# Performance work log

Measured on AMD Instinct MI355X. Metric: run time of the kernel, lower is better.

Reference implementation:

```python
import jax, jax.numpy as jnp
import numpy as np

B, H, S, D = 2, 16, 2048, 128


def setup_inputs() -> dict:
    key = jax.random.key(0)
    kq, kk, kv, km = jax.random.split(key, 4)
    query = jax.random.normal(kq, (B, H, S, D), dtype=jnp.float32)
    k_ = jax.random.normal(kk, (B, H, S, D), dtype=jnp.float32)
    value = jax.random.normal(kv, (B, H, S, D), dtype=jnp.float32)
    # per-sample context mask (attn_mask * learned mask scalar -> continuous floats)
    ctx_mask = jax.random.uniform(km, (B, S), dtype=jnp.float32)
    return {"query": query, "key": k_, "value": value, "ctx_mask": ctx_mask}


def reference(query, key, value, ctx_mask):
    # Faithful port of the monkey-patched GPT-Neo _attn (eval mode, no
    # attention_mask / head_mask, dropout = identity).
    q = query.astype(jnp.float32)
    k = key.astype(jnp.float32)
    # GPT-Neo: no 1/sqrt(d) scaling
    scores = jnp.einsum("bhqd,bhkd->bhqk", q, k)  # [B,H,S,S] fp32
    q_len, k_len = scores.shape[-2], scores.shape[-1]
    causal = jnp.tril(jnp.ones((q_len, k_len), dtype=bool))  # bias buffer slice
    mask_value = jnp.finfo(scores.dtype).min
    scores = jnp.where(causal, scores, mask_value)
    attn = jax.nn.softmax(scores, axis=-1).astype(value.dtype)
    # per-sample ctx_mask multiply over the key axis (post-softmax!)
    attn = attn * ctx_mask[:, None, None, :]
    out = jnp.einsum("bhqk,bhkd->bhqd", attn, value)
    return out
```

## Files before the change

### kernel.cpp

```cpp
#include <hip/hip_runtime.h>
#include <stdint.h>


#define S_LEN 2048
#define DIM 128
#define QTILE 128
#define KTILE 32
#define LOG2E 1.44269504088896340736f
#define NEG_BIG (-3.0e38f)

typedef _Float16 half8 __attribute__((ext_vector_type(8)));
typedef float f32x16 __attribute__((ext_vector_type(16)));

union U4H8 { uint4 u; half8 h; };

static __device__ __forceinline__ unsigned int pkh2(float a, float b) {
  unsigned short ua = __builtin_bit_cast(unsigned short, (_Float16)a);
  unsigned short ub = __builtin_bit_cast(unsigned short, (_Float16)b);
  return (unsigned int)ua | ((unsigned int)ub << 16);
}

static __device__ __forceinline__ void split8(const float* x, uint4& uh, uint4& ul) {
  unsigned int h[4], l[4];
#pragma unroll
  for (int i = 0; i < 4; ++i) {
    float a = x[2 * i], b = x[2 * i + 1];
    _Float16 ha = (_Float16)a, hb = (_Float16)b;
    float ra = a - (float)ha, rb = b - (float)hb;
    h[i] = (unsigned int)__builtin_bit_cast(unsigned short, ha)
         | ((unsigned int)__builtin_bit_cast(unsigned short, hb) << 16);
    l[i] = (unsigned int)__builtin_bit_cast(unsigned short, (_Float16)ra)
         | ((unsigned int)__builtin_bit_cast(unsigned short, (_Float16)rb) << 16);
  }
  uh = make_uint4(h[0], h[1], h[2], h[3]);
  ul = make_uint4(l[0], l[1], l[2], l[3]);
}

__global__ __launch_bounds__(256, 2) void attn_fwd(
    const float* __restrict__ Q, const float* __restrict__ K,
    const float* __restrict__ V, const float* __restrict__ CM,
    float* __restrict__ O) {
  __shared__ uint4 sKhi[512];
  __shared__ uint4 sKlo[512];
  __shared__ uint4 sVt[512];

  const int tid = (int)threadIdx.x;
  const int lane = tid & 63;
  const int wv = tid >> 6;
  const int l31 = lane & 31;
  const int hif = lane >> 5;

  const int pid = (int)blockIdx.x;
  const int t16 = pid >> 5;
  const int qt = (t16 < 8) ? t16 : (23 - t16);
  const int bh = pid & 31;
  const int b = bh >> 4;

  const float* Qb = Q + (size_t)bh * (S_LEN * DIM);
  const float* Kb = K + (size_t)bh * (S_LEN * DIM);
  const float* Vb = V + (size_t)bh * (S_LEN * DIM);
  const float* CMb = CM + (size_t)b * S_LEN;
  float* Ob = O + (size_t)bh * (S_LEN * DIM);

  const int qb = qt * QTILE + wv * 32;
  const int q = qb + l31;
  const int kdiag = qb >> 5;
  const int nkt = 4 * qt + 4;

  uint4 qh[8], ql[8];
  {
    const float* qrow = Qb + (size_t)q * DIM;
#pragma unroll
    for (int ko = 0; ko < 8; ++ko) {
      const int d0 = ko * 16 + hif * 8;
      float4 f0 = *(const float4*)(qrow + d0);
      float4 f1 = *(const float4*)(qrow + d0 + 4);
      float x[8] = {f0.x * LOG2E, f0.y * LOG2E, f0.z * LOG2E, f0.w * LOG2E,
                    f1.x * LOG2E, f1.y * LOG2E, f1.z * LOG2E, f1.w * LOG2E};
      split8(x, qh[ko], ql[ko]);
    }
  }

  f32x16 accO[4];
#pragma unroll
  for (int dt = 0; dt < 4; ++dt)
#pragma unroll
    for (int i = 0; i < 16; ++i) accO[dt][i] = 0.f;
  float m = NEG_BIG;
  float lsum = 0.f;

  for (int kt = 0; kt < nkt; ++kt) {
    __syncthreads();
    const int kb = kt * KTILE;

#pragma unroll
    for (int cc = 0; cc < 2; ++cc) {
      const int c = tid + cc * 256;
      const int row = c >> 4;
      const int col8 = c & 15;
      const float* src = Kb + (size_t)(kb + row) * DIM + col8 * 8;
      float4 f0 = *(const float4*)src;
      float4 f1 = *(const float4*)(src + 4);
      float x[8] = {f0.x, f0.y, f0.z, f0.w, f1.x, f1.y, f1.z, f1.w};
      uint4 uh, ul;
      split8(x, uh, ul);
      const int idx = row * 16 + (col8 ^ (row & 7));
      sKhi[idx] = uh;
      sKlo[idx] = ul;
    }
#pragma unroll
    for (int cc = 0; cc < 2; ++cc) {
      const int c = tid + cc * 256;
      const int kc = c >> 7;
      const int d = c & 127;
      unsigned int pk[4];
#pragma unroll
      for (int i = 0; i < 4; ++i) {
        const int k0 = kb + kc * 8 + 2 * i;
        float a = Vb[(size_t)k0 * DIM + d] * CMb[k0];
        float bb = Vb[(size_t)(k0 + 1) * DIM + d] * CMb[k0 + 1];
        pk[i] = pkh2(a, bb);
      }
      sVt[c] = make_uint4(pk[0], pk[1], pk[2], pk[3]);
    }
    __syncthreads();

    if (kt > kdiag) continue;

    f32x16 s;
#pragma unroll
    for (int i = 0; i < 16; ++i) s[i] = 0.f;
    const int rbase = l31 * 16;
    const int sw = l31 & 7;
#pragma unroll
    for (int ko = 0; ko < 8; ++ko) {
      const int idx = rbase + ((2 * ko + hif) ^ sw);
      U4H8 ah, al, bhq, blq;
      ah.u = sKhi[idx];
      al.u = sKlo[idx];
      bhq.u = qh[ko];
      blq.u = ql[ko];
      s = __builtin_amdgcn_mfma_f32_32x32x16_f16(al.h, bhq.h, s, 0, 0, 0);
      s = __builtin_amdgcn_mfma_f32_32x32x16_f16(ah.h, blq.h, s, 0, 0, 0);
      s = __builtin_amdgcn_mfma_f32_32x32x16_f16(ah.h, bhq.h, s, 0, 0, 0);
    }

    if (kt == kdiag) {
#pragma unroll
      for (int r = 0; r < 16; ++r) {
        const int crow = (r & 3) + 8 * (r >> 2) + 4 * hif;
        if (crow > l31) s[r] = NEG_BIG;
      }
    }

    float pmax = s[0];
#pragma unroll
    for (int r = 1; r < 16; ++r) pmax = fmaxf(pmax, s[r]);
    pmax = fmaxf(pmax, __shfl_xor(pmax, 32));

    if (__any(pmax > m + 8.0f)) {
      const float mnew = fmaxf(m, pmax);
      const float sc = exp2f(m - mnew);
      m = mnew;
      lsum *= sc;
#pragma unroll
      for (int dt = 0; dt < 4; ++dt)
#pragma unroll
        for (int i = 0; i < 16; ++i) accO[dt][i] *= sc;
    }

    float p[16];
    float psum = 0.f;
#pragma unroll
    for (int r = 0; r < 16; ++r) {
      p[r] = exp2f(s[r] - m);
      psum += p[r];
    }
    psum += __shfl_xor(psum, 32);
    lsum += psum;

#pragma unroll
    for (int ko = 0; ko < 2; ++ko) {
      const unsigned int a0 = pkh2(p[8 * ko + 0], p[8 * ko + 1]);
      const unsigned int a1 = pkh2(p[8 * ko + 2], p[8 * ko + 3]);
      const unsigned int b0 = pkh2(p[8 * ko + 4], p[8 * ko + 5]);
      const unsigned int b1 = pkh2(p[8 * ko + 6], p[8 * ko + 7]);
      const unsigned int s0 = hif ? a0 : b0;
      const unsigned int s1 = hif ? a1 : b1;
      const unsigned int r0 = __shfl_xor(s0, 32);
      const unsigned int r1 = __shfl_xor(s1, 32);
      U4H8 pf;
      if (hif) pf.u = make_uint4(r0, r1, b0, b1);
      else     pf.u = make_uint4(a0, a1, r0, r1);
#pragma unroll
      for (int dt = 0; dt < 4; ++dt) {
        U4H8 vf;
        vf.u = sVt[(2 * ko + hif) * 128 + dt * 32 + l31];
        accO[dt] = __builtin_amdgcn_mfma_f32_32x32x16_f16(vf.h, pf.h, accO[dt], 0, 0, 0);
      }
    }
  }

  const float rinv = 1.0f / lsum;
  float* orow = Ob + (size_t)q * DIM;
#pragma unroll
  for (int dt = 0; dt < 4; ++dt) {
#pragma unroll
    for (int g = 0; g < 4; ++g) {
      float4 o;
      o.x = accO[dt][4 * g + 0] * rinv;
      o.y = accO[dt][4 * g + 1] * rinv;
      o.z = accO[dt][4 * g + 2] * rinv;
      o.w = accO[dt][4 * g + 3] * rinv;
      *(float4*)(orow + dt * 32 + g * 8 + 4 * hif) = o;
    }
  }
}

extern "C" void kernel_launch(void* const* d_in, const int* in_sizes, int n_in,
                              void* d_out, int out_size, void* d_ws, size_t ws_size,
                              hipStream_t stream) {
  const float* Q = (const float*)d_in[0];
  const float* K = (const float*)d_in[1];
  const float* V = (const float*)d_in[2];
  const float* CM = (const float*)d_in[3];
  float* Out = (float*)d_out;
  hipLaunchKernelGGL(attn_fwd, dim3(512), dim3(256), 0, stream, Q, K, V, CM, Out);
}
```

Before: 295.1 us.

## Prepack K/V tiles in workspace and double-buffer async loads into LDS

Adds a prepack kernel that splits K into hi/lo fp16 and multiplies V by ctx_mask, transposing it to fp16, once per tile into a workspace. The attention kernel then streams the prepacked tiles into double-buffered LDS with global_load_lds while computing, and raises wave priority around the MFMA blocks. Each query-tile block no longer repeats the conversion work, and the loads overlap with compute. In exchange it adds an extra kernel launch, a workspace round trip through HBM, and double the LDS per block. It falls back to the old kernel if the workspace is too small.

```diff
diff --git a/kernel.cpp b/kernel.cpp
--- a/kernel.cpp
+++ b/kernel.cpp
@@ -6,11 +6,17 @@
 #define DIM 128
 #define QTILE 128
 #define KTILE 32
+#define NKT_TOT 64
+#define TILE_U4 1536
+#define WS_NEED ((size_t)32 * NKT_TOT * TILE_U4 * 16)
 #define LOG2E 1.44269504088896340736f
 #define NEG_BIG (-3.0e38f)
 
 typedef _Float16 half8 __attribute__((ext_vector_type(8)));
 typedef float f32x16 __attribute__((ext_vector_type(16)));
+typedef unsigned int u32;
+typedef __attribute__((address_space(3))) u32 lds_u32;
+typedef const __attribute__((address_space(1))) u32 glb_u32;
 
 union U4H8 { uint4 u; half8 h; };
 
@@ -36,13 +42,61 @@
   ul = make_uint4(l[0], l[1], l[2], l[3]);
 }
 
-__global__ __launch_bounds__(256, 2) void attn_fwd(
-    const float* __restrict__ Q, const float* __restrict__ K,
-    const float* __restrict__ V, const float* __restrict__ CM,
+__global__ __launch_bounds__(256) void prepack(
+    const float* __restrict__ K, const float* __restrict__ V,
+    const float* __restrict__ CM, uint4* __restrict__ ws) {
+  const int bid = (int)blockIdx.x;
+  const int bh = bid >> 6;
+  const int kt = bid & 63;
+  const int b = bh >> 4;
+  const int kb = kt * KTILE;
+  const int tid = (int)threadIdx.x;
+  const float* Kb = K + (size_t)bh * (S_LEN * DIM);
+  const float* Vb = V + (size_t)bh * (S_LEN * DIM);
+  const float* CMb = CM + (size_t)b * S_LEN;
+  uint4* tile = ws + (size_t)bid * TILE_U4;
+
+#pragma unroll
+  for (int cc = 0; cc < 2; ++cc) {
+    const int c = tid + cc * 256;
+    const int row = c >> 4;
+    const int col8 = c & 15;
+    const float* src = Kb + (size_t)(kb + row) * DIM + col8 * 8;
+    float4 f0 = *(const float4*)src;
+    float4 f1 = *(const float4*)(src + 4);
+    float x[8] = {f0.x, f0.y, f0.z, f0.w, f1.x, f1.y, f1.z, f1.w};
+    uint4 uh, ul;
+    split8(x, uh, ul);
+    const int idx = row * 16 + (col8 ^ (row & 7));
+    tile[idx] = uh;
+    tile[512 + idx] = ul;
+  }
+
+  const int kc = tid >> 6;
+  const int half = (tid >> 5) & 1;
+  const int dgrp = tid & 31;
+  const int k0 = kb + kc * 8 + half * 4;
+  float cm[4];
+  float vv[4][4];
+#pragma unroll
+  for (int j = 0; j < 4; ++j) {
+    cm[j] = CMb[k0 + j];
+    *(float4*)vv[j] = *(const float4*)(Vb + (size_t)(k0 + j) * DIM + dgrp * 4);
+  }
+#pragma unroll
+  for (int i = 0; i < 4; ++i) {
+    uint2 w;
+    w.x = pkh2(vv[0][i] * cm[0], vv[1][i] * cm[1]);
+    w.y = pkh2(vv[2][i] * cm[2], vv[3][i] * cm[3]);
+    char* dst = (char*)(tile + 1024 + kc * 128 + dgrp * 4 + i) + half * 8;
+    *(uint2*)dst = w;
+  }
+}
+
+__global__ __launch_bounds__(256, 2) void attn_fwd2(
+    const float* __restrict__ Q, const uint4* __restrict__ ws,
     float* __restrict__ O) {
-  __shared__ uint4 sKhi[512];
-  __shared__ uint4 sKlo[512];
-  __shared__ uint4 sVt[512];
+  __shared__ uint4 sBuf[2][TILE_U4];
 
   const int tid = (int)threadIdx.x;
   const int lane = tid & 63;
@@ -54,18 +108,24 @@
   const int t16 = pid >> 5;
   const int qt = (t16 < 8) ? t16 : (23 - t16);
   const int bh = pid & 31;
-  const int b = bh >> 4;
 
   const float* Qb = Q + (size_t)bh * (S_LEN * DIM);
-  const float* Kb = K + (size_t)bh * (S_LEN * DIM);
-  const float* Vb = V + (size_t)bh * (S_LEN * DIM);
-  const float* CMb = CM + (size_t)b * S_LEN;
   float* Ob = O + (size_t)bh * (S_LEN * DIM);
+  const uint4* wsbh = ws + (size_t)bh * NKT_TOT * TILE_U4;
 
   const int qb = qt * QTILE + wv * 32;
   const int q = qb + l31;
   const int kdiag = qb >> 5;
   const int nkt = 4 * qt + 4;
+
+  {
+    const uint4* src = wsbh;
+#pragma unroll
+    for (int j = 0; j < 6; ++j) {
+      __builtin_amdgcn_global_load_lds((glb_u32*)(src + tid + j * 256),
+                                       (lds_u32*)&sBuf[0][tid + j * 256], 16, 0, 0);
+    }
+  }
 
   uint4 qh[8], ql[8];
   {
@@ -89,10 +149,174 @@
   float m = NEG_BIG;
   float lsum = 0.f;
 
+  __syncthreads();
+
+  int cur = 0;
+  for (int kt = 0; kt < nkt; ++kt) {
+    if (kt + 1 < nkt) {
+      const uint4* src = wsbh + (size_t)(kt + 1) * TILE_U4;
+#pragma unroll
+      for (int j = 0; j < 6; ++j) {
+        __builtin_amdgcn_global_load_lds((glb_u32*)(src + tid + j * 256),
+                                         (lds_u32*)&sBuf[cur ^ 1][tid + j * 256], 16, 0, 0);
+      }
+    }
+
+    if (kt <= kdiag) {
+      f32x16 s;
+#pragma unroll
+      for (int i = 0; i < 16; ++i) s[i] = 0.f;
+      const int rbase = l31 * 16;
+      const int sw = l31 & 7;
+      __builtin_amdgcn_s_setprio(1);
+#pragma unroll
+      for (int ko = 0; ko < 8; ++ko) {
+        const int idx = rbase + ((2 * ko + hif) ^ sw);
+        U4H8 ah, al, bhq, blq;
+        ah.u = sBuf[cur][idx];
+        al.u = sBuf[cur][512 + idx];
+        bhq.u = qh[ko];
+        blq.u = ql[ko];
+        s = __builtin_amdgcn_mfma_f32_32x32x16_f16(al.h, bhq.h, s, 0, 0, 0);
+        s = __builtin_amdgcn_mfma_f32_32x32x16_f16(ah.h, blq.h, s, 0, 0, 0);
+        s = __builtin_amdgcn_mfma_f32_32x32x16_f16(ah.h, bhq.h, s, 0, 0, 0);
+      }
+      __builtin_amdgcn_s_setprio(0);
+
+      if (kt == kdiag) {
+#pragma unroll
+        for (int r = 0; r < 16; ++r) {
+          const int crow = (r & 3) + 8 * (r >> 2) + 4 * hif;
+          if (crow > l31) s[r] = NEG_BIG;
+        }
+      }
+
+      float pmax = s[0];
+#pragma unroll
+      for (int r = 1; r < 16; ++r) pmax = fmaxf(pmax, s[r]);
+      pmax = fmaxf(pmax, __shfl_xor(pmax, 32));
+
+      if (__any(pmax > m + 8.0f)) {
+        const float mnew = fmaxf(m, pmax);
+        const float sc = exp2f(m - mnew);
+        m = mnew;
+        lsum *= sc;
+#pragma unroll
+        for (int dt = 0; dt < 4; ++dt)
+#pragma unroll
+          for (int i = 0; i < 16; ++i) accO[dt][i] *= sc;
+      }
+
+      float p[16];
+      float psum = 0.f;
+#pragma unroll
+      for (int r = 0; r < 16; ++r) {
+        p[r] = exp2f(s[r] - m);
+        psum += p[r];
+      }
+      psum += __shfl_xor(psum, 32);
+      lsum += psum;
+
+      __builtin_amdgcn_s_setprio(1);
+#pragma unroll
+      for (int ko = 0; ko < 2; ++ko) {
+        const unsigned int a0 = pkh2(p[8 * ko + 0], p[8 * ko + 1]);
+        const unsigned int a1 = pkh2(p[8 * ko + 2], p[8 * ko + 3]);
+        const unsigned int b0 = pkh2(p[8 * ko + 4], p[8 * ko + 5]);
+        const unsigned int b1 = pkh2(p[8 * ko + 6], p[8 * ko + 7]);
+        const unsigned int s0 = hif ? a0 : b0;
+        const unsigned int s1 = hif ? a1 : b1;
+        const unsigned int r0 = __shfl_xor(s0, 32);
+        const unsigned int r1 = __shfl_xor(s1, 32);
+        U4H8 pf;
+        if (hif) pf.u = make_uint4(r0, r1, b0, b1);
+        else     pf.u = make_uint4(a0, a1, r0, r1);
+#pragma unroll
+        for (int dt = 0; dt < 4; ++dt) {
+          U4H8 vf;
+          vf.u = sBuf[cur][1024 + (2 * ko + hif) * 128 + dt * 32 + l31];
+          accO[dt] = __builtin_amdgcn_mfma_f32_32x32x16_f16(vf.h, pf.h, accO[dt], 0, 0, 0);
+        }
+      }
+      __builtin_amdgcn_s_setprio(0);
+    }
+
+    __syncthreads();
+    cur ^= 1;
+  }
+
+  const float rinv = 1.0f / lsum;
+  float* orow = Ob + (size_t)q * DIM;
+#pragma unroll
+  for (int dt = 0; dt < 4; ++dt) {
+#pragma unroll
+    for (int g = 0; g < 4; ++g) {
+      float4 o;
+      o.x = accO[dt][4 * g + 0] * rinv;
+      o.y = accO[dt][4 * g + 1] * rinv;
+      o.z = accO[dt][4 * g + 2] * rinv;
+      o.w = accO[dt][4 * g + 3] * rinv;
+      *(float4*)(orow + dt * 32 + g * 8 + 4 * hif) = o;
+    }
+  }
+}
+
+__global__ __launch_bounds__(256, 2) void attn_fwd_fb(
+    const float* __restrict__ Q, const float* __restrict__ K,
+    const float* __restrict__ V, const float* __restrict__ CM,
+    float* __restrict__ O) {
+  __shared__ uint4 sKhi[512];
+  __shared__ uint4 sKlo[512];
+  __shared__ uint4 sVt[512];
+
+  const int tid = (int)threadIdx.x;
+  const int lane = tid & 63;
+  const int wv = tid >> 6;
+  const int l31 = lane & 31;
+  const int hif = lane >> 5;
+
+  const int pid = (int)blockIdx.x;
+  const int t16 = pid >> 5;
+  const int qt = (t16 < 8) ? t16 : (23 - t16);
+  const int bh = pid & 31;
+  const int b = bh >> 4;
+
+  const float* Qb = Q + (size_t)bh * (S_LEN * DIM);
+  const float* Kb = K + (size_t)bh * (S_LEN * DIM);
+  const float* Vb = V + (size_t)bh * (S_LEN * DIM);
+  const float* CMb = CM + (size_t)b * S_LEN;
+  float* Ob = O + (size_t)bh * (S_LEN * DIM);
+
+  const int qb = qt * QTILE + wv * 32;
+  const int q = qb + l31;
+  const int kdiag = qb >> 5;
+  const int nkt = 4 * qt + 4;
+
+  uint4 qh[8], ql[8];
+  {
+    const float* qrow = Qb + (size_t)q * DIM;
+#pragma unroll
+    for (int ko = 0; ko < 8; ++ko) {
+      const int d0 = ko * 16 + hif * 8;
+      float4 f0 = *(const float4*)(qrow + d0);
+      float4 f1 = *(const float4*)(qrow + d0 + 4);
+      float x[8] = {f0.x * LOG2E, f0.y * LOG2E, f0.z * LOG2E, f0.w * LOG2E,
+                    f1.x * LOG2E, f1.y * LOG2E, f1.z * LOG2E, f1.w * LOG2E};
+      split8(x, qh[ko], ql[ko]);
+    }
+  }
+
+  f32x16 accO[4];
+#pragma unroll
+  for (int dt = 0; dt < 4; ++dt)
+#pragma unroll
+    for (int i = 0; i < 16; ++i) accO[dt][i] = 0.f;
+  float m = NEG_BIG;
+  float lsum = 0.f;
+
   for (int kt = 0; kt < nkt; ++kt) {
     __syncthreads();
     const int kb = kt * KTILE;
-
 #pragma unroll
     for (int cc = 0; cc < 2; ++cc) {
       const int c = tid + cc * 256;
@@ -225,5 +449,12 @@
   const float* V = (const float*)d_in[2];
   const float* CM = (const float*)d_in[3];
   float* Out = (float*)d_out;
-  hipLaunchKernelGGL(attn_fwd, dim3(512), dim3(256), 0, stream, Q, K, V, CM, Out);
-}
+
+  if (ws_size >= WS_NEED) {
+    uint4* ws = (uint4*)d_ws;
+    hipLaunchKernelGGL(prepack, dim3(32 * NKT_TOT), dim3(256), 0, stream, K, V, CM, ws);
+    hipLaunchKernelGGL(attn_fwd2, dim3(512), dim3(256), 0, stream, Q, (const uint4*)ws, Out);
+  } else {
+    hipLaunchKernelGGL(attn_fwd_fb, dim3(512), dim3(256), 0, stream, Q, K, V, CM, Out);
+  }
+}
```

Result: faster. 257.1 us (-12.9%).
